# Performance work log

Hardware: AMD Instinct MI355X
Metric: run time of the kernel (lower is better)

Reference implementation:

```python
import jax, jax.numpy as jnp
import numpy as np

N_NODES = 100000
N_EDGES = 1600000
NUM_FEATURES = 512
NHID = 256
CHEB_K = 6


def setup_inputs() -> dict:
    key = jax.random.key(0)
    ks = jax.random.split(key, 12)
    x = jax.random.normal(ks[0], (N_NODES, NUM_FEATURES), dtype=jnp.float32)
    edge_index = jax.random.randint(ks[1], (2, N_EDGES), 0, N_NODES, dtype=jnp.int64)
    edge_weight = jax.random.uniform(ks[2], (N_EDGES,), dtype=jnp.float32)
    s = 1.0 / np.sqrt(NUM_FEATURES)
    W1 = jax.random.uniform(ks[3], (NUM_FEATURES, NHID), jnp.float32, -s, s)
    b1 = jnp.zeros((NHID,), jnp.float32)
    s2 = 1.0 / np.sqrt(NHID)
    Wc = jax.random.uniform(ks[4], (CHEB_K, NHID, NHID // 2), jnp.float32, -s2, s2)
    bc = jnp.zeros((NHID // 2,), jnp.float32)
    s3 = 1.0 / np.sqrt(NHID // 2)
    W_out = jax.random.uniform(ks[5], (NHID // 2, 1), jnp.float32, -s3, s3)
    W_root = jax.random.uniform(ks[6], (NHID // 2, 1), jnp.float32, -s3, s3)
    b3 = jnp.zeros((1,), jnp.float32)
    return {"x": x, "edge_index": edge_index, "edge_weight": edge_weight,
            "W1": W1, "b1": b1, "Wc": Wc, "bc": bc,
            "W_out": W_out, "W_root": W_root, "b3": b3}


def _safe_rsqrt(d):
    return jnp.where(d > 0, jax.lax.rsqrt(jnp.where(d > 0, d, 1.0)), 0.0)


def _gcn_conv(x, src, dst, ew, W, b, n):
    # GCNConv: add self-loops (weight 1), sym-normalize, then aggregate x @ W.
    loop = jnp.arange(n)
    src2 = jnp.concatenate([src, loop])
    dst2 = jnp.concatenate([dst, loop])
    ew2 = jnp.concatenate([ew, jnp.ones((n,), ew.dtype)])
    deg = jax.ops.segment_sum(ew2, dst2, num_segments=n)
    dis = _safe_rsqrt(deg)
    norm = dis[src2] * ew2 * dis[dst2]                     # [E+N]
    h = x @ W                                              # [N, out]
    out = jax.ops.segment_sum(h[src2] * norm[:, None], dst2, num_segments=n)
    return out + b


def _cheb_conv(x, src, dst, ew, Wc, bc, n):
    # ChebConv (sym norm, lambda_max=2): L_hat = -D^{-1/2} A D^{-1/2} (diag 0).
    deg = jax.ops.segment_sum(ew, dst, num_segments=n)
    dis = _safe_rsqrt(deg)
    wn = -(dis[src] * ew * dis[dst])                        # [E]

    def lmv(h):  # L_hat @ h
        return jax.ops.segment_sum(h[src] * wn[:, None], dst, num_segments=n)

    Tx0 = x
    out = Tx0 @ Wc[0]
    Tx1 = lmv(x)
    out = out + Tx1 @ Wc[1]
    for k in range(2, Wc.shape[0]):
        Tx2 = 2.0 * lmv(Tx1) - Tx0
        out = out + Tx2 @ Wc[k]
        Tx0, Tx1 = Tx1, Tx2
    return out + bc


def _cluster_gcn_conv(x, src, dst, W_out, W_root, b, n):
    # ClusterGCNConv (diag_lambda=0): out = (D^{-1}(A+I) x) W_out + b + x W_root.
    loop = jnp.arange(n)
    src2 = jnp.concatenate([src, loop])
    dst2 = jnp.concatenate([dst, loop])
    deg = jax.ops.segment_sum(jnp.ones_like(dst2, dtype=x.dtype), dst2, num_segments=n)
    w = (1.0 / jnp.maximum(deg, 1.0))[dst2]                 # [E+N]
    agg = jax.ops.segment_sum(x[src2] * w[:, None], dst2, num_segments=n)
    return agg @ W_out + b + x @ W_root


def reference(x, edge_index, edge_weight, W1, b1, Wc, bc, W_out, W_root, b3):
    n = x.shape[0]
    src, dst = edge_index[0], edge_index[1]
    h = _gcn_conv(x, src, dst, edge_weight, W1, b1, n)
    h = jax.nn.relu(h)
    # dropout is identity in eval mode
    h = _cheb_conv(h, src, dst, edge_weight, Wc, bc, n)
    h = jax.nn.relu(h)
    features = h
    out = _cluster_gcn_conv(h, src, dst, W_out, W_root, b3, n)
    return (out.reshape(-1), features)
```

## Files before the change

### kernel.cpp

```cpp
#include <hip/hip_runtime.h>
#include <cstdint>
#include <cstddef>

typedef __attribute__((ext_vector_type(8))) short bf16x8;
typedef __attribute__((ext_vector_type(4))) float f32x4;

static inline int ceil_div(int a, int b){ return (a + b - 1) / b; }

struct HL { short h, l; };
__device__ inline HL split2(float a){
  unsigned u = __float_as_uint(a);
  unsigned hb = (u + 0x8000u) & 0xFFFF0000u;
  float r = a - __uint_as_float(hb);
  HL o;
  o.h = (short)(hb >> 16);
  o.l = (short)((__float_as_uint(r) + 0x8000u) >> 16);
  return o;
}

__device__ inline unsigned short f2b(float f){
  unsigned u = __float_as_uint(f);
  unsigned r = u + 0x7FFFu + ((u >> 16) & 1u);
  return (unsigned short)(r >> 16);
}
__device__ inline float b2f(unsigned short s){
  return __uint_as_float((unsigned)s << 16);
}

__global__ __launch_bounds__(256) void k_detect(const int* __restrict__ ei32, int E, int* __restrict__ flag){
  int t = blockIdx.x * 256 + threadIdx.x;
  if (t < 4096) {
    long long idx = 2LL * t + 1;
    if (idx < 2LL * E && ei32[idx] != 0) atomicOr(flag, 1);
  }
}

__global__ __launch_bounds__(256) void k_count(const void* __restrict__ ei, int E,
                                               const int* __restrict__ flag, int* __restrict__ cnt){
  int e = blockIdx.x * 256 + threadIdx.x;
  if (e >= E) return;
  int dst = (*flag) ? ((const int*)ei)[(size_t)E + e]
                    : (int)((const long long*)ei)[(size_t)E + e];
  atomicAdd(&cnt[dst], 1);
}

__global__ __launch_bounds__(256) void k_scan_part(const int* __restrict__ cnt, int* __restrict__ bsum, int N){
  int base = blockIdx.x * 1024 + threadIdx.x * 4;
  int s = 0;
  if (base + 4 <= N){
    int4 v = *(const int4*)(cnt + base);
    s = v.x + v.y + v.z + v.w;
  } else {
    for (int i = base; i < N; ++i) s += cnt[i];
  }
#pragma unroll
  for (int off = 32; off; off >>= 1) s += __shfl_xor(s, off);
  __shared__ int ws[4];
  if ((threadIdx.x & 63) == 0) ws[threadIdx.x >> 6] = s;
  __syncthreads();
  if (threadIdx.x == 0) bsum[blockIdx.x] = ws[0] + ws[1] + ws[2] + ws[3];
}

__global__ __launch_bounds__(1024) void k_scan_bsum(int* __restrict__ bsum, int nb){
  __shared__ int sh[1024];
  int t = threadIdx.x;
  int v = (t < nb) ? bsum[t] : 0;
  sh[t] = v; __syncthreads();
  for (int off = 1; off < 1024; off <<= 1){
    int u = (t >= off) ? sh[t - off] : 0;
    __syncthreads();
    sh[t] += u;
    __syncthreads();
  }
  if (t < nb) bsum[t] = sh[t] - v;
}

__global__ __launch_bounds__(256) void k_scan_write(const int* __restrict__ cnt, const int* __restrict__ bsum,
                                                    int* __restrict__ row_ptr, int* __restrict__ cursor,
                                                    int N, int E){
  int t = threadIdx.x;
  int base = blockIdx.x * 1024 + t * 4;
  int v0 = 0, v1 = 0, v2 = 0, v3 = 0;
  if (base + 4 <= N){
    int4 v = *(const int4*)(cnt + base);
    v0 = v.x; v1 = v.y; v2 = v.z; v3 = v.w;
  } else {
    if (base + 0 < N) v0 = cnt[base + 0];
    if (base + 1 < N) v1 = cnt[base + 1];
    if (base + 2 < N) v2 = cnt[base + 2];
    if (base + 3 < N) v3 = cnt[base + 3];
  }
  int s = v0 + v1 + v2 + v3;
  int lane = t & 63;
  int inc = s;
#pragma unroll
  for (int off = 1; off < 64; off <<= 1){
    int u = __shfl_up(inc, off);
    if (lane >= off) inc += u;
  }
  __shared__ int ws[4];
  if (lane == 63) ws[t >> 6] = inc;
  __syncthreads();
  int wid = t >> 6;
  int woff = 0;
  for (int i = 0; i < wid; ++i) woff += ws[i];
  int exc = bsum[blockIdx.x] + woff + inc - s;
  int p0 = exc, p1 = p0 + v0, p2 = p1 + v1, p3 = p2 + v2;
  if (base + 0 < N){ row_ptr[base + 0] = p0; cursor[base + 0] = p0; }
  if (base + 1 < N){ row_ptr[base + 1] = p1; cursor[base + 1] = p1; }
  if (base + 2 < N){ row_ptr[base + 2] = p2; cursor[base + 2] = p2; }
  if (base + 3 < N){ row_ptr[base + 3] = p3; cursor[base + 3] = p3; }
  if (blockIdx.x == 0 && t == 0) row_ptr[N] = E;
}

__global__ __launch_bounds__(256) void k_fill(const void* __restrict__ ei, const float* __restrict__ ew, int E,
                                              const int* __restrict__ flag, int* __restrict__ cursor,
                                              int* __restrict__ csr_src, float* __restrict__ csr_ew){
  int e = blockIdx.x * 256 + threadIdx.x;
  if (e >= E) return;
  int src, dst;
  if (*flag){ src = ((const int*)ei)[e]; dst = ((const int*)ei)[(size_t)E + e]; }
  else      { src = (int)((const long long*)ei)[e]; dst = (int)((const long long*)ei)[(size_t)E + e]; }
  int pos = atomicAdd(&cursor[dst], 1);
  csr_src[pos] = src;
  csr_ew[pos] = ew[e];
}

__global__ __launch_bounds__(256) void k_degrees(const int* __restrict__ row_ptr, const float* __restrict__ csr_ew,
                                                 float* __restrict__ dis1, float* __restrict__ dis2,
                                                 float* __restrict__ invw, int N){
  int r = blockIdx.x * 256 + threadIdx.x;
  if (r >= N) return;
  int e0 = row_ptr[r], e1 = row_ptr[r + 1];
  float s = 0.f;
  for (int e = e0; e < e1; ++e) s += csr_ew[e];
  dis1[r] = rsqrtf(s + 1.0f);
  dis2[r] = (s > 0.0f) ? rsqrtf(s) : 0.0f;
  invw[r] = 1.0f / (float)(e1 - e0 + 1);
}

__global__ __launch_bounds__(256) void k_norm(const int* __restrict__ csr_src, const float* __restrict__ csr_ew,
                                              const float* __restrict__ dis1, const float* __restrict__ dis2,
                                              float* __restrict__ w_gcn, float* __restrict__ w_cheb, int E){
  int e = blockIdx.x * 256 + threadIdx.x;
  if (e >= E) return;
  int s = csr_src[e];
  float w = csr_ew[e];
  w_gcn[e]  = w * dis1[s];
  w_cheb[e] = w * dis2[s];
}

__global__ __launch_bounds__(256) void k_prep_w(const float* __restrict__ W, short* __restrict__ Wh,
                                                short* __restrict__ Wl, int K, int N){
  int idx = blockIdx.x * 256 + threadIdx.x;
  if (idx >= K * N) return;
  int n = idx / K, k = idx - n * K;
  HL s = split2(W[(size_t)k * N + n]);
  Wh[idx] = s.h; Wl[idx] = s.l;
}

__global__ __launch_bounds__(256) void k_prep_wc(const float* __restrict__ Wc, short* __restrict__ Wh){
  int idx = blockIdx.x * 256 + threadIdx.x;
  if (idx >= 768 * 256) return;
  int n = idx >> 8, k = idx & 255;
  Wh[idx] = (short)f2b(Wc[(size_t)(n >> 7) * 256 * 128 + (size_t)k * 128 + (n & 127)]);
}

__global__ __launch_bounds__(256) void k_gemm_mfma(
    const float* __restrict__ A,
    const short* __restrict__ Bh, const short* __restrict__ Bl,
    unsigned short* __restrict__ Cb,
    int M, int Ncols, int K)
{
  __shared__ short Ah[128][40];
  __shared__ short Bhs[128][40];
  __shared__ short Bls[128][40];
  int m0 = blockIdx.x * 128, n0 = blockIdx.y * 128;
  int t = threadIdx.x;
  int lane = t & 63, wid = t >> 6;
  int wr = wid >> 1, wc = wid & 1;
  int fr = lane & 15, fq = lane >> 4;
  int srow = t >> 1, skh = (t & 1) << 4;

  f32x4 acc[4][4];
#pragma unroll
  for (int i = 0; i < 4; ++i)
#pragma unroll
    for (int j = 0; j < 4; ++j) acc[i][j] = (f32x4){0.f, 0.f, 0.f, 0.f};

  bool aval = (m0 + srow) < M;
  const float* Aptr = A + (size_t)(m0 + srow) * K + skh;
  const short* Bhp = Bh + (size_t)(n0 + srow) * K + skh;
  const short* Blp = Bl + (size_t)(n0 + srow) * K + skh;

  for (int k0 = 0; k0 < K; k0 += 32){
    __syncthreads();
    float av[16];
    if (aval){
      const float4* ap = (const float4*)(Aptr + k0);
      float4 a0 = ap[0], a1 = ap[1], a2 = ap[2], a3 = ap[3];
      av[0]=a0.x; av[1]=a0.y; av[2]=a0.z; av[3]=a0.w;
      av[4]=a1.x; av[5]=a1.y; av[6]=a1.z; av[7]=a1.w;
      av[8]=a2.x; av[9]=a2.y; av[10]=a2.z; av[11]=a2.w;
      av[12]=a3.x; av[13]=a3.y; av[14]=a3.z; av[15]=a3.w;
    } else {
#pragma unroll
      for (int i = 0; i < 16; ++i) av[i] = 0.f;
    }
    bf16x8 h0, h1;
#pragma unroll
    for (int i = 0; i < 8; ++i) h0[i] = (short)f2b(av[i]);
#pragma unroll
    for (int i = 0; i < 8; ++i) h1[i] = (short)f2b(av[8 + i]);
    *(bf16x8*)&Ah[srow][skh]     = h0;
    *(bf16x8*)&Ah[srow][skh + 8] = h1;
    {
      const bf16x8* bp = (const bf16x8*)(Bhp + k0);
      *(bf16x8*)&Bhs[srow][skh]     = bp[0];
      *(bf16x8*)&Bhs[srow][skh + 8] = bp[1];
      const bf16x8* cp = (const bf16x8*)(Blp + k0);
      *(bf16x8*)&Bls[srow][skh]     = cp[0];
      *(bf16x8*)&Bls[srow][skh + 8] = cp[1];
    }
    __syncthreads();
    bf16x8 afh[4], bfh[4], bfl[4];
#pragma unroll
    for (int m = 0; m < 4; ++m){
      int r = wr * 64 + m * 16 + fr;
      afh[m] = *(const bf16x8*)&Ah[r][fq * 8];
    }
#pragma unroll
    for (int n = 0; n < 4; ++n){
      int r = wc * 64 + n * 16 + fr;
      bfh[n] = *(const bf16x8*)&Bhs[r][fq * 8];
      bfl[n] = *(const bf16x8*)&Bls[r][fq * 8];
    }
#pragma unroll
    for (int m = 0; m < 4; ++m)
#pragma unroll
      for (int n = 0; n < 4; ++n){
        acc[m][n] = __builtin_amdgcn_mfma_f32_16x16x32_bf16(afh[m], bfh[n], acc[m][n], 0, 0, 0);
        acc[m][n] = __builtin_amdgcn_mfma_f32_16x16x32_bf16(afh[m], bfl[n], acc[m][n], 0, 0, 0);
      }
  }
#pragma unroll
  for (int m = 0; m < 4; ++m){
#pragma unroll
    for (int n = 0; n < 4; ++n){
      int col = n0 + wc * 64 + n * 16 + fr;
#pragma unroll
      for (int r = 0; r < 4; ++r){
        int row = m0 + wr * 64 + m * 16 + fq * 4 + r;
        if (row < M){
          Cb[(size_t)row * Ncols + col] = f2b(acc[m][n][r]);
        }
      }
    }
  }
}

__global__ __launch_bounds__(256) void k_gemm_mfma2(
    const unsigned short* __restrict__ Ahg, const unsigned short* __restrict__ Alg,
    const short* __restrict__ Bh,
    unsigned short* __restrict__ Cb,
    int M, int Ncols, int K, int nbm)
{
  __shared__ short Ah[128][40];
  __shared__ short Al[128][40];
  __shared__ short Bhs[128][40];
  int bid = blockIdx.x;
  int g = bid & 7, j = bid >> 3;
  int m_tile = g + 8 * (j / 6);
  int n_tile = j - 6 * (j / 6);
  if (m_tile >= nbm) return;
  int m0 = m_tile * 128, n0 = n_tile * 128;
  int t = threadIdx.x;
  int lane = t & 63, wid = t >> 6;
  int wr = wid >> 1, wc = wid & 1;
  int fr = lane & 15, fq = lane >> 4;
  int srow = t >> 1, skh = (t & 1) << 4;

  f32x4 acc[4][4];
#pragma unroll
  for (int i = 0; i < 4; ++i)
#pragma unroll
    for (int jj = 0; jj < 4; ++jj) acc[i][jj] = (f32x4){0.f, 0.f, 0.f, 0.f};

  bool aval = (m0 + srow) < M;
  const unsigned short* Ahp = Ahg + (size_t)(m0 + srow) * K + skh;
  const unsigned short* Alp = Alg + (size_t)(m0 + srow) * K + skh;
  const short* Bhp = Bh + (size_t)(n0 + srow) * K + skh;

  for (int k0 = 0; k0 < K; k0 += 32){
    __syncthreads();
    if (aval){
      const bf16x8* ah = (const bf16x8*)(Ahp + k0);
      *(bf16x8*)&Ah[srow][skh]     = ah[0];
      *(bf16x8*)&Ah[srow][skh + 8] = ah[1];
      const bf16x8* al = (const bf16x8*)(Alp + k0);
      *(bf16x8*)&Al[srow][skh]     = al[0];
      *(bf16x8*)&Al[srow][skh + 8] = al[1];
    } else {
      bf16x8 z = (bf16x8){0,0,0,0,0,0,0,0};
      *(bf16x8*)&Ah[srow][skh] = z; *(bf16x8*)&Ah[srow][skh + 8] = z;
      *(bf16x8*)&Al[srow][skh] = z; *(bf16x8*)&Al[srow][skh + 8] = z;
    }
    {
      const bf16x8* bp = (const bf16x8*)(Bhp + k0);
      *(bf16x8*)&Bhs[srow][skh]     = bp[0];
      *(bf16x8*)&Bhs[srow][skh + 8] = bp[1];
    }
    __syncthreads();
    bf16x8 afh[4], afl[4], bfh[4];
#pragma unroll
    for (int m = 0; m < 4; ++m){
      int r = wr * 64 + m * 16 + fr;
      afh[m] = *(const bf16x8*)&Ah[r][fq * 8];
      afl[m] = *(const bf16x8*)&Al[r][fq * 8];
    }
#pragma unroll
    for (int n = 0; n < 4; ++n){
      int r = wc * 64 + n * 16 + fr;
      bfh[n] = *(const bf16x8*)&Bhs[r][fq * 8];
    }
#pragma unroll
    for (int m = 0; m < 4; ++m)
#pragma unroll
      for (int n = 0; n < 4; ++n){
        acc[m][n] = __builtin_amdgcn_mfma_f32_16x16x32_bf16(afh[m], bfh[n], acc[m][n], 0, 0, 0);
        acc[m][n] = __builtin_amdgcn_mfma_f32_16x16x32_bf16(afl[m], bfh[n], acc[m][n], 0, 0, 0);
      }
  }
#pragma unroll
  for (int m = 0; m < 4; ++m){
#pragma unroll
    for (int n = 0; n < 4; ++n){
      int col = n0 + wc * 64 + n * 16 + fr;
#pragma unroll
      for (int r = 0; r < 4; ++r){
        int row = m0 + wr * 64 + m * 16 + fq * 4 + r;
        if (row < M){
          Cb[(size_t)row * Ncols + col] = f2b(acc[m][n][r]);
        }
      }
    }
  }
}

__global__ __launch_bounds__(256) void k_gcn_agg(
    const unsigned short* __restrict__ h0b,
    const int* __restrict__ csr_src, const float* __restrict__ w_gcn,
    const int* __restrict__ row_ptr, const float* __restrict__ dis1,
    const float* __restrict__ b1,
    unsigned short* __restrict__ h1h, unsigned short* __restrict__ h1l, int N){
  int lane = threadIdx.x & 63;
  int r = blockIdx.x * 4 + (threadIdx.x >> 6);
  if (r >= N) return;
  float dr = dis1[r];
  ushort4 sv = ((const ushort4*)(h0b + (size_t)r * 256))[lane];
  float4 inner = make_float4(b2f(sv.x) * dr, b2f(sv.y) * dr, b2f(sv.z) * dr, b2f(sv.w) * dr);
  int e0 = row_ptr[r], e1 = row_ptr[r + 1];
  int e = e0;
  for (; e + 8 <= e1; e += 8){
    int   si[8]; float wi[8]; ushort4 vi[8];
#pragma unroll
    for (int q = 0; q < 8; ++q){ si[q] = csr_src[e + q]; wi[q] = w_gcn[e + q]; }
#pragma unroll
    for (int q = 0; q < 8; ++q) vi[q] = ((const ushort4*)(h0b + (size_t)si[q] * 256))[lane];
#pragma unroll
    for (int q = 0; q < 8; ++q){
      inner.x = fmaf(wi[q], b2f(vi[q].x), inner.x);
      inner.y = fmaf(wi[q], b2f(vi[q].y), inner.y);
      inner.z = fmaf(wi[q], b2f(vi[q].z), inner.z);
      inner.w = fmaf(wi[q], b2f(vi[q].w), inner.w);
    }
  }
  for (; e < e1; ++e){
    int s = csr_src[e];
    float w = w_gcn[e];
    ushort4 v = ((const ushort4*)(h0b + (size_t)s * 256))[lane];
    inner.x = fmaf(w, b2f(v.x), inner.x); inner.y = fmaf(w, b2f(v.y), inner.y);
    inner.z = fmaf(w, b2f(v.z), inner.z); inner.w = fmaf(w, b2f(v.w), inner.w);
  }
  float4 bb = ((const float4*)b1)[lane];
  float4 o;
  o.x = fmaxf(fmaf(inner.x, dr, bb.x), 0.f);
  o.y = fmaxf(fmaf(inner.y, dr, bb.y), 0.f);
  o.z = fmaxf(fmaf(inner.z, dr, bb.z), 0.f);
  o.w = fmaxf(fmaf(inner.w, dr, bb.w), 0.f);
  HL sx = split2(o.x), sy = split2(o.y), sz = split2(o.z), sw = split2(o.w);
  ushort4 hi; hi.x = (unsigned short)sx.h; hi.y = (unsigned short)sy.h; hi.z = (unsigned short)sz.h; hi.w = (unsigned short)sw.h;
  ushort4 lo; lo.x = (unsigned short)sx.l; lo.y = (unsigned short)sy.l; lo.z = (unsigned short)sz.l; lo.w = (unsigned short)sw.l;
  ((ushort4*)(h1h + (size_t)r * 256))[lane] = hi;
  ((ushort4*)(h1l + (size_t)r * 256))[lane] = lo;
}

__global__ __launch_bounds__(256) void k_cheb_spmm2(
    const unsigned short* __restrict__ Ck, int ckstride,
    const unsigned short* __restrict__ sub16, int substride,
    const float* __restrict__ subf,
    const unsigned short* __restrict__ srcb, int sstride,
    float* __restrict__ dst, unsigned short* __restrict__ dstb,
    const int* __restrict__ csr_src, const float* __restrict__ w_cheb,
    const int* __restrict__ row_ptr, const float* __restrict__ dis2, float coef, int N){
  int lane = threadIdx.x & 63;
  int r = blockIdx.x * 4 + (threadIdx.x >> 6);
  if (r >= N) return;
  float2 inner = make_float2(0.f, 0.f);
  int e0 = row_ptr[r], e1 = row_ptr[r + 1];
  int e = e0;
  for (; e + 8 <= e1; e += 8){
    int si[8]; float wi[8]; unsigned vi[8];
#pragma unroll
    for (int q = 0; q < 8; ++q){ si[q] = csr_src[e + q]; wi[q] = w_cheb[e + q]; }
#pragma unroll
    for (int q = 0; q < 8; ++q) vi[q] = ((const unsigned*)(srcb + (size_t)si[q] * sstride))[lane];
#pragma unroll
    for (int q = 0; q < 8; ++q){
      inner.x = fmaf(wi[q], __uint_as_float(vi[q] << 16), inner.x);
      inner.y = fmaf(wi[q], __uint_as_float(vi[q] & 0xFFFF0000u), inner.y);
    }
  }
  for (; e < e1; ++e){
    int s = csr_src[e];
    float w = w_cheb[e];
    unsigned v = ((const unsigned*)(srcb + (size_t)s * sstride))[lane];
    inner.x = fmaf(w, __uint_as_float(v << 16), inner.x);
    inner.y = fmaf(w, __uint_as_float(v & 0xFFFF0000u), inner.y);
  }
  float c = coef * dis2[r];
  unsigned ckv = ((const unsigned*)(Ck + (size_t)r * ckstride))[lane];
  float rx = fmaf(c, inner.x, __uint_as_float(ckv << 16));
  float ry = fmaf(c, inner.y, __uint_as_float(ckv & 0xFFFF0000u));
  if (sub16){
    unsigned sv = ((const unsigned*)(sub16 + (size_t)r * substride))[lane];
    rx -= __uint_as_float(sv << 16);
    ry -= __uint_as_float(sv & 0xFFFF0000u);
  }
  if (subf){
    float2 s2 = ((const float2*)(subf + (size_t)r * 128))[lane];
    rx -= s2.x;
    ry -= s2.y;
  }
  ((float2*)(dst + (size_t)r * 128))[lane] = make_float2(rx, ry);
  if (dstb){
    unsigned pk = (unsigned)f2b(rx) | ((unsigned)f2b(ry) << 16);
    ((unsigned*)(dstb + (size_t)r * 128))[lane] = pk;
  }
}

__global__ __launch_bounds__(256) void k_spmm_final(
    const unsigned short* __restrict__ Ck, int ckstride,
    const float* __restrict__ subf,
    const unsigned short* __restrict__ srcb, int sstride,
    const float* __restrict__ bc, const float* __restrict__ W_out, const float* __restrict__ W_root,
    float* __restrict__ feat, float* __restrict__ p, float* __restrict__ wr,
    const int* __restrict__ csr_src, const float* __restrict__ w_cheb,
    const int* __restrict__ row_ptr, const float* __restrict__ dis2, float coef, int N){
  int lane = threadIdx.x & 63;
  int r = blockIdx.x * 4 + (threadIdx.x >> 6);
  if (r >= N) return;
  float2 inner = make_float2(0.f, 0.f);
  int e0 = row_ptr[r], e1 = row_ptr[r + 1];
  int e = e0;
  for (; e + 8 <= e1; e += 8){
    int si[8]; float wi[8]; unsigned vi[8];
#pragma unroll
    for (int q = 0; q < 8; ++q){ si[q] = csr_src[e + q]; wi[q] = w_cheb[e + q]; }
#pragma unroll
    for (int q = 0; q < 8; ++q) vi[q] = ((const unsigned*)(srcb + (size_t)si[q] * sstride))[lane];
#pragma unroll
    for (int q = 0; q < 8; ++q){
      inner.x = fmaf(wi[q], __uint_as_float(vi[q] << 16), inner.x);
      inner.y = fmaf(wi[q], __uint_as_float(vi[q] & 0xFFFF0000u), inner.y);
    }
  }
  for (; e < e1; ++e){
    int s = csr_src[e];
    float w = w_cheb[e];
    unsigned v = ((const unsigned*)(srcb + (size_t)s * sstride))[lane];
    inner.x = fmaf(w, __uint_as_float(v << 16), inner.x);
    inner.y = fmaf(w, __uint_as_float(v & 0xFFFF0000u), inner.y);
  }
  float c = coef * dis2[r];
  unsigned ckv = ((const unsigned*)(Ck + (size_t)r * ckstride))[lane];
  float rx = fmaf(c, inner.x, __uint_as_float(ckv << 16));
  float ry = fmaf(c, inner.y, __uint_as_float(ckv & 0xFFFF0000u));
  float2 s2 = ((const float2*)(subf + (size_t)r * 128))[lane];
  rx -= s2.x;
  ry -= s2.y;
  float2 bb = ((const float2*)bc)[lane];
  rx = fmaxf(rx + bb.x, 0.f);
  ry = fmaxf(ry + bb.y, 0.f);
  ((float2*)(feat + (size_t)r * 128))[lane] = make_float2(rx, ry);
  float2 wo = ((const float2*)W_out)[lane];
  float2 wrt = ((const float2*)W_root)[lane];
  float pp = rx * wo.x + ry * wo.y;
  float rr = rx * wrt.x + ry * wrt.y;
#pragma unroll
  for (int off = 32; off; off >>= 1){
    pp += __shfl_xor(pp, off);
    rr += __shfl_xor(rr, off);
  }
  if (lane == 0){ p[r] = pp; wr[r] = rr; }
}

__global__ __launch_bounds__(256) void k_out(const float* __restrict__ p, const float* __restrict__ wr,
    const float* __restrict__ invw, const int* __restrict__ csr_src, const int* __restrict__ row_ptr,
    const float* __restrict__ b3, float* __restrict__ out, int N){
  int r = blockIdx.x * 256 + threadIdx.x;
  if (r >= N) return;
  float s = p[r];
  int e0 = row_ptr[r], e1 = row_ptr[r + 1];
  int e = e0;
  float acc[8] = {0.f,0.f,0.f,0.f,0.f,0.f,0.f,0.f};
  for (; e + 8 <= e1; e += 8){
    int si[8];
#pragma unroll
    for (int q = 0; q < 8; ++q) si[q] = csr_src[e + q];
#pragma unroll
    for (int q = 0; q < 8; ++q) acc[q] += p[si[q]];
  }
  for (; e < e1; ++e) acc[0] += p[csr_src[e]];
  s += ((acc[0]+acc[1])+(acc[2]+acc[3])) + ((acc[4]+acc[5])+(acc[6]+acc[7]));
  out[r] = invw[r] * s + wr[r] + b3[0];
}

extern "C" void kernel_launch(void* const* d_in, const int* in_sizes, int n_in,
                              void* d_out, int out_size, void* d_ws, size_t ws_size,
                              hipStream_t stream){
  const float* x      = (const float*)d_in[0];
  const void*  ei     = d_in[1];
  const float* ew     = (const float*)d_in[2];
  const float* W1     = (const float*)d_in[3];
  const float* b1     = (const float*)d_in[4];
  const float* Wc     = (const float*)d_in[5];
  const float* bc     = (const float*)d_in[6];
  const float* W_out  = (const float*)d_in[7];
  const float* W_root = (const float*)d_in[8];
  const float* b3     = (const float*)d_in[9];
  const int N = in_sizes[0] / 512;
  const int E = in_sizes[2];

  char* w = (char*)d_ws;
  auto alloc = [&](size_t bytes)->void*{ void* r = (void*)w; w += (bytes + 255) & ~(size_t)255; return r; };
  unsigned short* h1h = (unsigned short*)alloc((size_t)N * 256 * 2 * 2);
  unsigned short* h1l = h1h + (size_t)N * 256;
  float* B0 = (float*)h1h;
  float* B1 = B0 + (size_t)N * 128;
  float* B2 = (float*)alloc((size_t)N * 128 * 4);
  unsigned short* CC  = (unsigned short*)alloc((size_t)N * 768 * 2);
  unsigned short* h0b = (unsigned short*)alloc((size_t)N * 256 * 2);
  unsigned short* Bb0 = h0b;
  unsigned short* Bb1 = h0b + (size_t)N * 128;
  float* csr_ew  = (float*)alloc((size_t)E * 4);
  float* w_gcn   = (float*)alloc((size_t)E * 4);
  float* w_cheb  = (float*)alloc((size_t)E * 4);
  int*   csr_src = (int*)  alloc((size_t)E * 4);
  int*   row_ptr = (int*)  alloc((size_t)(N + 1) * 4);
  int*   cursor  = (int*)  alloc((size_t)N * 4);
  int*   cnt     = (int*)  alloc((size_t)N * 4);
  int*   bsum    = (int*)  alloc((size_t)1024 * 4);
  float* dis1    = (float*)alloc((size_t)N * 4);
  float* dis2    = (float*)alloc((size_t)N * 4);
  float* invw    = (float*)alloc((size_t)N * 4);
  float* pbuf    = (float*)alloc((size_t)N * 4);
  float* wrbuf   = (float*)alloc((size_t)N * 4);
  short* W1t_h   = (short*)alloc((size_t)512 * 256 * 2);
  short* W1t_l   = (short*)alloc((size_t)512 * 256 * 2);
  short* Wct_h   = (short*)alloc((size_t)768 * 256 * 2);
  int*   flag    = (int*)  alloc(256);

  hipMemsetAsync(cnt, 0, (size_t)N * 4, stream);
  hipMemsetAsync(flag, 0, 4, stream);

  k_detect<<<16, 256, 0, stream>>>((const int*)ei, E, flag);
  k_count<<<ceil_div(E, 256), 256, 0, stream>>>(ei, E, flag, cnt);
  int nb = ceil_div(N, 1024);
  k_scan_part<<<nb, 256, 0, stream>>>(cnt, bsum, N);
  k_scan_bsum<<<1, 1024, 0, stream>>>(bsum, nb);
  k_scan_write<<<nb, 256, 0, stream>>>(cnt, bsum, row_ptr, cursor, N, E);
  k_fill<<<ceil_div(E, 256), 256, 0, stream>>>(ei, ew, E, flag, cursor, csr_src, csr_ew);
  k_degrees<<<ceil_div(N, 256), 256, 0, stream>>>(row_ptr, csr_ew, dis1, dis2, invw, N);
  k_norm<<<ceil_div(E, 256), 256, 0, stream>>>(csr_src, csr_ew, dis1, dis2, w_gcn, w_cheb, E);

  k_prep_w<<<ceil_div(512 * 256, 256), 256, 0, stream>>>(W1, W1t_h, W1t_l, 512, 256);
  k_prep_wc<<<ceil_div(768 * 256, 256), 256, 0, stream>>>(Wc, Wct_h);

  k_gemm_mfma<<<dim3(ceil_div(N, 128), 2), 256, 0, stream>>>(x, W1t_h, W1t_l, h0b, N, 256, 512);
  k_gcn_agg<<<ceil_div(N, 4), 256, 0, stream>>>(h0b, csr_src, w_gcn, row_ptr, dis1, b1, h1h, h1l, N);

  int nbm = ceil_div(N, 128);
  int grid2 = 8 * 6 * ceil_div(nbm, 8);
  k_gemm_mfma2<<<grid2, 256, 0, stream>>>(h1h, h1l, Wct_h, CC, N, 768, 256, nbm);

  auto spmm = [&](const unsigned short* Ck, const unsigned short* s16, int s16s, const float* sf,
                  const unsigned short* src, int ss, float* dst, unsigned short* dstb, float coef){
    k_cheb_spmm2<<<ceil_div(N, 4), 256, 0, stream>>>(Ck, 768, s16, s16s, sf, src, ss, dst, dstb,
        csr_src, w_cheb, row_ptr, dis2, coef, N);
  };
  spmm(CC + 4*128, nullptr, 0, nullptr, CC + 5*128, 768, B0, Bb0, -2.f);
  spmm(CC + 3*128, CC + 5*128, 768, nullptr, Bb0, 128, B1, Bb1, -2.f);
  spmm(CC + 2*128, nullptr, 0, B0, Bb1, 128, B2, Bb0, -2.f);
  spmm(CC + 1*128, nullptr, 0, B1, Bb0, 128, B0, Bb1, -2.f);

  float* out  = (float*)d_out;
  float* feat = out + N;
  k_spmm_final<<<ceil_div(N, 4), 256, 0, stream>>>(CC + 0*128, 768, B2, Bb1, 128,
      bc, W_out, W_root, feat, pbuf, wrbuf, csr_src, w_cheb, row_ptr, dis2, -1.f, N);
  k_out<<<ceil_div(N, 256), 256, 0, stream>>>(pbuf, wrbuf, invw, csr_src, row_ptr, b3, out, N);
}
```

Measured before the change: 1.069 ms.

## Prefetch A tiles in GEMMs, swizzle GEMM1 grid, write compact C5 copy

Both MFMA GEMMs now load the next K-slice of A into registers while the current slice is computed, moving the barrier to the end of the iteration so global latency overlaps with MFMA work. The first GEMM uses the same grouped 1D block ordering as the second, with 8 M-tiles sharing N-tiles, to improve L2 reuse. The second GEMM also writes the last output slice into a compact 128-wide buffer (reusing B2 storage), so the first two SpMM passes gather contiguous 256-byte rows instead of strided slices of a 768-wide matrix. This costs extra registers for the prefetch, an extra store pass in the GEMM, and relies on B2 not being live until the third SpMM.

```diff
diff --git a/kernel.cpp b/kernel.cpp
--- a/kernel.cpp
+++ b/kernel.cpp
@@ -170,12 +170,17 @@
     const float* __restrict__ A,
     const short* __restrict__ Bh, const short* __restrict__ Bl,
     unsigned short* __restrict__ Cb,
-    int M, int Ncols, int K)
+    int M, int Ncols, int K, int nbm)
 {
   __shared__ short Ah[128][40];
   __shared__ short Bhs[128][40];
   __shared__ short Bls[128][40];
-  int m0 = blockIdx.x * 128, n0 = blockIdx.y * 128;
+  int bid = blockIdx.x;
+  int g = bid & 7, j = bid >> 3;
+  int m_tile = g + 8 * (j >> 1);
+  int n_tile = j & 1;
+  if (m_tile >= nbm) return;
+  int m0 = m_tile * 128, n0 = n_tile * 128;
   int t = threadIdx.x;
   int lane = t & 63, wid = t >> 6;
   int wr = wid >> 1, wc = wid & 1;
@@ -186,32 +191,25 @@
 #pragma unroll
   for (int i = 0; i < 4; ++i)
 #pragma unroll
-    for (int j = 0; j < 4; ++j) acc[i][j] = (f32x4){0.f, 0.f, 0.f, 0.f};
+    for (int jj = 0; jj < 4; ++jj) acc[i][jj] = (f32x4){0.f, 0.f, 0.f, 0.f};
 
   bool aval = (m0 + srow) < M;
   const float* Aptr = A + (size_t)(m0 + srow) * K + skh;
   const short* Bhp = Bh + (size_t)(n0 + srow) * K + skh;
   const short* Blp = Bl + (size_t)(n0 + srow) * K + skh;
 
+  float4 a0, a1, a2, a3;
+  if (aval){
+    const float4* ap = (const float4*)Aptr;
+    a0 = ap[0]; a1 = ap[1]; a2 = ap[2]; a3 = ap[3];
+  } else a0 = a1 = a2 = a3 = make_float4(0.f, 0.f, 0.f, 0.f);
+
   for (int k0 = 0; k0 < K; k0 += 32){
-    __syncthreads();
-    float av[16];
-    if (aval){
-      const float4* ap = (const float4*)(Aptr + k0);
-      float4 a0 = ap[0], a1 = ap[1], a2 = ap[2], a3 = ap[3];
-      av[0]=a0.x; av[1]=a0.y; av[2]=a0.z; av[3]=a0.w;
-      av[4]=a1.x; av[5]=a1.y; av[6]=a1.z; av[7]=a1.w;
-      av[8]=a2.x; av[9]=a2.y; av[10]=a2.z; av[11]=a2.w;
-      av[12]=a3.x; av[13]=a3.y; av[14]=a3.z; av[15]=a3.w;
-    } else {
-#pragma unroll
-      for (int i = 0; i < 16; ++i) av[i] = 0.f;
-    }
     bf16x8 h0, h1;
-#pragma unroll
-    for (int i = 0; i < 8; ++i) h0[i] = (short)f2b(av[i]);
-#pragma unroll
-    for (int i = 0; i < 8; ++i) h1[i] = (short)f2b(av[8 + i]);
+    h0[0]=(short)f2b(a0.x); h0[1]=(short)f2b(a0.y); h0[2]=(short)f2b(a0.z); h0[3]=(short)f2b(a0.w);
+    h0[4]=(short)f2b(a1.x); h0[5]=(short)f2b(a1.y); h0[6]=(short)f2b(a1.z); h0[7]=(short)f2b(a1.w);
+    h1[0]=(short)f2b(a2.x); h1[1]=(short)f2b(a2.y); h1[2]=(short)f2b(a2.z); h1[3]=(short)f2b(a2.w);
+    h1[4]=(short)f2b(a3.x); h1[5]=(short)f2b(a3.y); h1[6]=(short)f2b(a3.z); h1[7]=(short)f2b(a3.w);
     *(bf16x8*)&Ah[srow][skh]     = h0;
     *(bf16x8*)&Ah[srow][skh + 8] = h1;
     {
@@ -223,6 +221,12 @@
       *(bf16x8*)&Bls[srow][skh + 8] = cp[1];
     }
     __syncthreads();
+    bool more = (k0 + 32) < K;
+    float4 n0v, n1v, n2v, n3v;
+    if (more && aval){
+      const float4* ap = (const float4*)(Aptr + k0 + 32);
+      n0v = ap[0]; n1v = ap[1]; n2v = ap[2]; n3v = ap[3];
+    } else n0v = n1v = n2v = n3v = make_float4(0.f, 0.f, 0.f, 0.f);
     bf16x8 afh[4], bfh[4], bfl[4];
 #pragma unroll
     for (int m = 0; m < 4; ++m){
@@ -242,6 +246,8 @@
         acc[m][n] = __builtin_amdgcn_mfma_f32_16x16x32_bf16(afh[m], bfh[n], acc[m][n], 0, 0, 0);
         acc[m][n] = __builtin_amdgcn_mfma_f32_16x16x32_bf16(afh[m], bfl[n], acc[m][n], 0, 0, 0);
       }
+    __syncthreads();
+    a0 = n0v; a1 = n1v; a2 = n2v; a3 = n3v;
   }
 #pragma unroll
   for (int m = 0; m < 4; ++m){
@@ -262,7 +268,7 @@
 __global__ __launch_bounds__(256) void k_gemm_mfma2(
     const unsigned short* __restrict__ Ahg, const unsigned short* __restrict__ Alg,
     const short* __restrict__ Bh,
-    unsigned short* __restrict__ Cb,
+    unsigned short* __restrict__ Cb, unsigned short* __restrict__ C5c,
     int M, int Ncols, int K, int nbm)
 {
   __shared__ short Ah[128][40];
@@ -291,26 +297,39 @@
   const unsigned short* Alp = Alg + (size_t)(m0 + srow) * K + skh;
   const short* Bhp = Bh + (size_t)(n0 + srow) * K + skh;
 
+  bf16x8 ch0, ch1, cl0, cl1;
+  if (aval){
+    const bf16x8* ah = (const bf16x8*)Ahp;
+    ch0 = ah[0]; ch1 = ah[1];
+    const bf16x8* al = (const bf16x8*)Alp;
+    cl0 = al[0]; cl1 = al[1];
+  } else {
+    bf16x8 z = (bf16x8){0,0,0,0,0,0,0,0};
+    ch0 = ch1 = cl0 = cl1 = z;
+  }
+
   for (int k0 = 0; k0 < K; k0 += 32){
-    __syncthreads();
-    if (aval){
-      const bf16x8* ah = (const bf16x8*)(Ahp + k0);
-      *(bf16x8*)&Ah[srow][skh]     = ah[0];
-      *(bf16x8*)&Ah[srow][skh + 8] = ah[1];
-      const bf16x8* al = (const bf16x8*)(Alp + k0);
-      *(bf16x8*)&Al[srow][skh]     = al[0];
-      *(bf16x8*)&Al[srow][skh + 8] = al[1];
-    } else {
-      bf16x8 z = (bf16x8){0,0,0,0,0,0,0,0};
-      *(bf16x8*)&Ah[srow][skh] = z; *(bf16x8*)&Ah[srow][skh + 8] = z;
-      *(bf16x8*)&Al[srow][skh] = z; *(bf16x8*)&Al[srow][skh + 8] = z;
-    }
+    *(bf16x8*)&Ah[srow][skh]     = ch0;
+    *(bf16x8*)&Ah[srow][skh + 8] = ch1;
+    *(bf16x8*)&Al[srow][skh]     = cl0;
+    *(bf16x8*)&Al[srow][skh + 8] = cl1;
     {
       const bf16x8* bp = (const bf16x8*)(Bhp + k0);
       *(bf16x8*)&Bhs[srow][skh]     = bp[0];
       *(bf16x8*)&Bhs[srow][skh + 8] = bp[1];
     }
     __syncthreads();
+    bool more = (k0 + 32) < K;
+    bf16x8 nh0, nh1, nl0, nl1;
+    if (more && aval){
+      const bf16x8* ah = (const bf16x8*)(Ahp + k0 + 32);
+      nh0 = ah[0]; nh1 = ah[1];
+      const bf16x8* al = (const bf16x8*)(Alp + k0 + 32);
+      nl0 = al[0]; nl1 = al[1];
+    } else {
+      bf16x8 z = (bf16x8){0,0,0,0,0,0,0,0};
+      nh0 = nh1 = nl0 = nl1 = z;
+    }
     bf16x8 afh[4], afl[4], bfh[4];
 #pragma unroll
     for (int m = 0; m < 4; ++m){
@@ -330,6 +349,8 @@
         acc[m][n] = __builtin_amdgcn_mfma_f32_16x16x32_bf16(afh[m], bfh[n], acc[m][n], 0, 0, 0);
         acc[m][n] = __builtin_amdgcn_mfma_f32_16x16x32_bf16(afl[m], bfh[n], acc[m][n], 0, 0, 0);
       }
+    __syncthreads();
+    ch0 = nh0; ch1 = nh1; cl0 = nl0; cl1 = nl1;
   }
 #pragma unroll
   for (int m = 0; m < 4; ++m){
@@ -340,7 +361,9 @@
       for (int r = 0; r < 4; ++r){
         int row = m0 + wr * 64 + m * 16 + fq * 4 + r;
         if (row < M){
-          Cb[(size_t)row * Ncols + col] = f2b(acc[m][n][r]);
+          unsigned short v = f2b(acc[m][n][r]);
+          Cb[(size_t)row * Ncols + col] = v;
+          if (n_tile == 5) C5c[(size_t)row * 128 + (col - 640)] = v;
         }
       }
     }
@@ -549,6 +572,7 @@
   float* B0 = (float*)h1h;
   float* B1 = B0 + (size_t)N * 128;
   float* B2 = (float*)alloc((size_t)N * 128 * 4);
+  unsigned short* C5c = (unsigned short*)B2;
   unsigned short* CC  = (unsigned short*)alloc((size_t)N * 768 * 2);
   unsigned short* h0b = (unsigned short*)alloc((size_t)N * 256 * 2);
   unsigned short* Bb0 = h0b;
@@ -587,20 +611,21 @@
   k_prep_w<<<ceil_div(512 * 256, 256), 256, 0, stream>>>(W1, W1t_h, W1t_l, 512, 256);
   k_prep_wc<<<ceil_div(768 * 256, 256), 256, 0, stream>>>(Wc, Wct_h);
 
-  k_gemm_mfma<<<dim3(ceil_div(N, 128), 2), 256, 0, stream>>>(x, W1t_h, W1t_l, h0b, N, 256, 512);
+  int nbm = ceil_div(N, 128);
+  int grid1 = 8 * 2 * ceil_div(nbm, 8);
+  k_gemm_mfma<<<grid1, 256, 0, stream>>>(x, W1t_h, W1t_l, h0b, N, 256, 512, nbm);
   k_gcn_agg<<<ceil_div(N, 4), 256, 0, stream>>>(h0b, csr_src, w_gcn, row_ptr, dis1, b1, h1h, h1l, N);
 
-  int nbm = ceil_div(N, 128);
   int grid2 = 8 * 6 * ceil_div(nbm, 8);
-  k_gemm_mfma2<<<grid2, 256, 0, stream>>>(h1h, h1l, Wct_h, CC, N, 768, 256, nbm);
+  k_gemm_mfma2<<<grid2, 256, 0, stream>>>(h1h, h1l, Wct_h, CC, C5c, N, 768, 256, nbm);
 
   auto spmm = [&](const unsigned short* Ck, const unsigned short* s16, int s16s, const float* sf,
                   const unsigned short* src, int ss, float* dst, unsigned short* dstb, float coef){
     k_cheb_spmm2<<<ceil_div(N, 4), 256, 0, stream>>>(Ck, 768, s16, s16s, sf, src, ss, dst, dstb,
         csr_src, w_cheb, row_ptr, dis2, coef, N);
   };
-  spmm(CC + 4*128, nullptr, 0, nullptr, CC + 5*128, 768, B0, Bb0, -2.f);
-  spmm(CC + 3*128, CC + 5*128, 768, nullptr, Bb0, 128, B1, Bb1, -2.f);
+  spmm(CC + 4*128, nullptr, 0, nullptr, C5c, 128, B0, Bb0, -2.f);
+  spmm(CC + 3*128, C5c, 128, nullptr, Bb0, 128, B1, Bb1, -2.f);
   spmm(CC + 2*128, nullptr, 0, B0, Bb1, 128, B2, Bb0, -2.f);
   spmm(CC + 1*128, nullptr, 0, B1, Bb0, 128, B0, Bb1, -2.f);
 
```

After: 1.049 ms. Within noise of the previous version (-1.8%).
